# Optimization experiments

Measured on AMD Instinct MI355X. Metric: run time of the kernel, lower is better.

Reference implementation:

```python
import jax, jax.numpy as jnp
import numpy as np


def pfaffian(A):
    """Pfaffian of even-dim skew-symmetric A via Parlett-Reid LTL^T (no pivoting).
    pf(A) = prod over elimination steps of the (k, k+1) pivot."""
    n = A.shape[0]
    ar = jnp.arange(n)

    def step(carry, i):
        A, pf = carry
        k = 2 * i
        pivot = A[k, k + 1]
        mask = ar > (k + 1)                      # rows/cols k+2:
        tau = jnp.where(mask, A[k, :], 0.0) / pivot
        col = jnp.where(mask, A[:, k + 1], 0.0)
        # rank-2 skew update of the trailing submatrix
        A = A + tau[:, None] * col[None, :] - col[:, None] * tau[None, :]
        return (A, pf * pivot), None

    (A, pf), _ = jax.lax.scan(step, (A, jnp.ones((), A.dtype)), jnp.arange(n // 2))
    return pf


def setup_inputs() -> dict:
    key = jax.random.key(0)
    k1, k2 = jax.random.split(key)
    N = 128          # nsites; Nparticle = N (spin system, one particle per site)
    B = 128          # batch of Monte-Carlo configurations
    x = jax.random.normal(k1, (B, N), jnp.float32)
    scale = np.float32(np.sqrt(np.e / N))
    F = jax.random.normal(k2, (N * (2 * N - 1),), jnp.float32) * scale
    return {"x": x, "F": F}


def reference(x, F):
    N = x.shape[-1]
    Nparticle = N
    twoN = 2 * N
    # scatter parameter vector into strict lower triangle, antisymmetrize
    F_full = jnp.zeros((twoN, twoN), F.dtype).at[jnp.tril_indices(twoN, -1)].set(F)
    F_full = F_full - F_full.T

    def single(xi):
        # spin system: up orbitals where x>0, down orbitals where x<=0
        occ = jnp.concatenate([xi > 0, xi <= 0])
        idx = jnp.flatnonzero(occ, size=Nparticle)
        A = F_full[idx[:, None], idx[None, :]]   # [Nparticle, Nparticle] gather
        return pfaffian(A)

    return jax.vmap(single)(x)
```

## Files before the change

### kernel.cpp

```cpp
#include <hip/hip_runtime.h>


#define POFF(i) ((i) + (((i) >> 5) << 2))
#define RL(v, l) __int_as_float(__builtin_amdgcn_readlane(__float_as_int(v), (l)))

__global__ __launch_bounds__(512) void pfaffian_kernel(
    const float* __restrict__ x,
    const float* __restrict__ F,
    float* __restrict__ out)
{
    const int b    = blockIdx.x;
    const int t    = threadIdx.x;
    const int lane = t & 63;
    const int wave = t >> 6;

    __shared__ int idx_sh[128];
    __shared__ int wtot[4];
    __shared__ __align__(16) float tauLDS[2][4][144];
    __shared__ __align__(16) float colLDS[2][4][144];
    __shared__ __align__(16) float rS[2][4][144];
    __shared__ __align__(16) float cS[2][4][144];

    if (t < 256) {
        const float xv  = x[b * 128 + (t & 127)];
        const bool  pos = xv > 0.0f;
        const bool  o   = (t < 128) ? pos : !pos;
        const unsigned long long mm = __ballot(o);
        const int rank = __popcll(mm & ((1ull << lane) - 1ull));
        if (lane == 63) wtot[wave] = rank + (o ? 1 : 0);
        __syncthreads();
        int off = 0;
#pragma unroll
        for (int w = 0; w < 4; ++w)
            if (w < wave) off += wtot[w];
        if (o) idx_sh[off + rank] = t;
    } else {
        __syncthreads();
    }
    __syncthreads();

    const int rg   = t >> 4;
    const int cg   = t & 15;
    const int row0 = rg << 2;
    const int col0 = cg << 3;
    const int prow = POFF(row0);
    const int pcol = POFF(col0);

    int ri[4], ci[8];
#pragma unroll
    for (int a = 0; a < 4; ++a) ri[a] = idx_sh[row0 + a];
#pragma unroll
    for (int c = 0; c < 8; ++c) ci[c] = idx_sh[col0 + c];

    float A[4][8];
#pragma unroll
    for (int a = 0; a < 4; ++a) {
        const int ii = ri[a];
#pragma unroll
        for (int c = 0; c < 8; ++c) {
            const int jj = ci[c];
            const int hi = ii > jj ? ii : jj;
            const int lo = ii > jj ? jj : ii;
            float v = (ii == jj) ? 0.0f : F[(hi * (hi - 1)) / 2 + lo];
            A[a][c] = (ii < jj) ? -v : v;
        }
    }

    auto stage = [&](int Pn, int st) {
        const int rgbase = 2 * Pn;
        if (rg == rgbase) {
            *(float4*)&rS[st][0][pcol]     = make_float4(A[0][0], A[0][1], A[0][2], A[0][3]);
            *(float4*)&rS[st][0][pcol + 4] = make_float4(A[0][4], A[0][5], A[0][6], A[0][7]);
            *(float4*)&rS[st][1][pcol]     = make_float4(A[2][0], A[2][1], A[2][2], A[2][3]);
            *(float4*)&rS[st][1][pcol + 4] = make_float4(A[2][4], A[2][5], A[2][6], A[2][7]);
        }
        if (rg == rgbase + 1) {
            *(float4*)&rS[st][2][pcol]     = make_float4(A[0][0], A[0][1], A[0][2], A[0][3]);
            *(float4*)&rS[st][2][pcol + 4] = make_float4(A[0][4], A[0][5], A[0][6], A[0][7]);
            *(float4*)&rS[st][3][pcol]     = make_float4(A[2][0], A[2][1], A[2][2], A[2][3]);
            *(float4*)&rS[st][3][pcol + 4] = make_float4(A[2][4], A[2][5], A[2][6], A[2][7]);
        }
        if (cg == Pn) {
            *(float4*)&cS[st][0][prow] = make_float4(A[0][1], A[1][1], A[2][1], A[3][1]);
            *(float4*)&cS[st][1][prow] = make_float4(A[0][3], A[1][3], A[2][3], A[3][3]);
            *(float4*)&cS[st][2][prow] = make_float4(A[0][5], A[1][5], A[2][5], A[3][5]);
            *(float4*)&cS[st][3][prow] = make_float4(A[0][7], A[1][7], A[2][7], A[3][7]);
        }
    };
    stage(0, 0);
    stage(1, 1);
    __syncthreads();

    float pf = 1.0f;

    auto crew2 = [&](int Pn, bool pre) {
        const int sv = Pn & 1;
        const int g0 = lane << 1;
        const int g1 = g0 + 1;
        const int pg = POFF(g0);
        float R[4][2], C[4][2];
#pragma unroll
        for (int j = 0; j < 4; ++j) {
            const float2 rv = *(const float2*)&rS[sv][j][pg];
            const float2 cv = *(const float2*)&cS[sv][j][pg];
            R[j][0] = rv.x; R[j][1] = rv.y;
            C[j][0] = cv.x; C[j][1] = cv.y;
        }
        if (pre) {
            const int svp  = sv ^ 1;
            const int base = POFF(8 * Pn);
            float4 Tq[4][2], Cq[4][2];
#pragma unroll
            for (int jp = 0; jp < 4; ++jp) {
                Tq[jp][0] = *(const float4*)&tauLDS[svp][jp][base];
                Tq[jp][1] = *(const float4*)&tauLDS[svp][jp][base + 4];
                Cq[jp][0] = *(const float4*)&colLDS[svp][jp][base];
                Cq[jp][1] = *(const float4*)&colLDS[svp][jp][base + 4];
            }
#pragma unroll
            for (int jp = 0; jp < 4; ++jp) {
                const float trA[4] = {Tq[jp][0].x, Tq[jp][0].z, Tq[jp][1].x, Tq[jp][1].z};
                const float crA[4] = {Cq[jp][0].x, Cq[jp][0].z, Cq[jp][1].x, Cq[jp][1].z};
                const float tcA[4] = {Tq[jp][0].y, Tq[jp][0].w, Tq[jp][1].y, Tq[jp][1].w};
                const float ccA[4] = {Cq[jp][0].y, Cq[jp][0].w, Cq[jp][1].y, Cq[jp][1].w};
                const float2 tpv = *(const float2*)&tauLDS[svp][jp][pg];
                const float2 cpv = *(const float2*)&colLDS[svp][jp][pg];
#pragma unroll
                for (int a = 0; a < 4; ++a) {
                    const float tau_r = trA[a];
                    const float col_r = crA[a];
                    R[a][0] = __fmaf_rn(-col_r, tpv.x,
                              __fmaf_rn(tau_r, cpv.x, R[a][0]));
                    R[a][1] = __fmaf_rn(-col_r, tpv.y,
                              __fmaf_rn(tau_r, cpv.y, R[a][1]));
                    const float tau_c = tcA[a];
                    const float col_c = ccA[a];
                    C[a][0] = __fmaf_rn(-cpv.x, tau_c,
                              __fmaf_rn(tpv.x, col_c, C[a][0]));
                    C[a][1] = __fmaf_rn(-cpv.y, tau_c,
                              __fmaf_rn(tpv.y, col_c, C[a][1]));
                }
            }
        }
        float TAU[4][2], CV[4][2];
#pragma unroll
        for (int j = 0; j < 4; ++j) {
            const int k = 8 * Pn + 2 * j;
            const float piv = RL(R[j][1], 4 * Pn + j);
            pf = __fmul_rn(pf, piv);
            TAU[j][0] = (g0 > k + 1) ? __fdiv_rn(R[j][0], piv) : 0.0f;
            TAU[j][1] = (g1 > k + 1) ? __fdiv_rn(R[j][1], piv) : 0.0f;
            CV[j][0]  = (g0 > k + 1) ? C[j][0] : 0.0f;
            CV[j][1]  = (g1 > k + 1) ? C[j][1] : 0.0f;
            *(float2*)&tauLDS[sv][j][pg] = make_float2(TAU[j][0], TAU[j][1]);
            *(float2*)&colLDS[sv][j][pg] = make_float2(CV[j][0], CV[j][1]);
#pragma unroll
            for (int j2 = j + 1; j2 < 4; ++j2) {
                const int ls = 4 * Pn + j2;
                const float tau_r = RL(TAU[j][0], ls);
                const float col_r = RL(CV[j][0], ls);
                R[j2][0] = __fmaf_rn(-col_r, TAU[j][0],
                           __fmaf_rn(tau_r, CV[j][0], R[j2][0]));
                R[j2][1] = __fmaf_rn(-col_r, TAU[j][1],
                           __fmaf_rn(tau_r, CV[j][1], R[j2][1]));
                const float tau_c = RL(TAU[j][1], ls);
                const float col_c = RL(CV[j][1], ls);
                C[j2][0] = __fmaf_rn(-CV[j][0], tau_c,
                           __fmaf_rn(TAU[j][0], col_c, C[j2][0]));
                C[j2][1] = __fmaf_rn(-CV[j][1], tau_c,
                           __fmaf_rn(TAU[j][1], col_c, C[j2][1]));
            }
        }
    };

    if (wave == 0) crew2(0, false);
    __syncthreads();

    for (int P = 0; P < 15; ++P) {
        if (wave >= 1 && 2 * wave > P) {
            const int sp = P & 1;
#pragma unroll
            for (int j = 0; j < 4; ++j) {
                const float4 trv = *(const float4*)&tauLDS[sp][j][prow];
                const float4 crv = *(const float4*)&colLDS[sp][j][prow];
                const float4 t0v = *(const float4*)&tauLDS[sp][j][pcol];
                const float4 t1v = *(const float4*)&tauLDS[sp][j][pcol + 4];
                const float4 c0v = *(const float4*)&colLDS[sp][j][pcol];
                const float4 c1v = *(const float4*)&colLDS[sp][j][pcol + 4];
                const float tr[4] = {trv.x, trv.y, trv.z, trv.w};
                const float cr[4] = {crv.x, crv.y, crv.z, crv.w};
                const float tc[8] = {t0v.x, t0v.y, t0v.z, t0v.w,
                                     t1v.x, t1v.y, t1v.z, t1v.w};
                const float cc[8] = {c0v.x, c0v.y, c0v.z, c0v.w,
                                     c1v.x, c1v.y, c1v.z, c1v.w};
#pragma unroll
                for (int a = 0; a < 4; ++a) {
#pragma unroll
                    for (int c = 0; c < 8; ++c) {
                        A[a][c] = __fmaf_rn(-cr[a], tc[c],
                                  __fmaf_rn(tr[a], cc[c], A[a][c]));
                    }
                }
            }
            if (P <= 13) stage(P + 2, P & 1);
        }
        if (wave == 0) crew2(P + 1, true);
        __syncthreads();
    }

    if (t == 0) out[b] = pf;
}

extern "C" void kernel_launch(void* const* d_in, const int* in_sizes, int n_in,
                              void* d_out, int out_size, void* d_ws, size_t ws_size,
                              hipStream_t stream) {
    const float* x = (const float*)d_in[0];
    const float* F = (const float*)d_in[1];
    float* out     = (float*)d_out;
    (void)in_sizes; (void)n_in; (void)out_size; (void)d_ws; (void)ws_size;

    pfaffian_kernel<<<128, 512, 0, stream>>>(x, F, out);
}
```

Baseline: 76.55 us.

## Double the panel width to eight pivots per barrier step

Widens each elimination panel from 4 to 8 pivot steps (16 columns), so the outer loop runs 7 barrier-separated iterations instead of 15. Shared staging buffers, the panel-factor routine in wave 0, and the trailing rank-2k update all process 8 tau/col vectors per step. This is meant to cut the number of __syncthreads and the per-step latency overhead. In exchange the serial panel work in wave 0 grows (more readlane chains and divisions) and more trailing work falls into whichever waves remain active.

```diff
diff --git a/kernel.cpp b/kernel.cpp
--- a/kernel.cpp
+++ b/kernel.cpp
@@ -16,10 +16,10 @@
 
     __shared__ int idx_sh[128];
     __shared__ int wtot[4];
-    __shared__ __align__(16) float tauLDS[2][4][144];
-    __shared__ __align__(16) float colLDS[2][4][144];
-    __shared__ __align__(16) float rS[2][4][144];
-    __shared__ __align__(16) float cS[2][4][144];
+    __shared__ __align__(16) float tauLDS[2][8][144];
+    __shared__ __align__(16) float colLDS[2][8][144];
+    __shared__ __align__(16) float rS[2][8][144];
+    __shared__ __align__(16) float cS[2][8][144];
 
     if (t < 256) {
         const float xv  = x[b * 128 + (t & 127)];
@@ -67,24 +67,24 @@
     }
 
     auto stage = [&](int Pn, int st) {
-        const int rgbase = 2 * Pn;
-        if (rg == rgbase) {
-            *(float4*)&rS[st][0][pcol]     = make_float4(A[0][0], A[0][1], A[0][2], A[0][3]);
-            *(float4*)&rS[st][0][pcol + 4] = make_float4(A[0][4], A[0][5], A[0][6], A[0][7]);
-            *(float4*)&rS[st][1][pcol]     = make_float4(A[2][0], A[2][1], A[2][2], A[2][3]);
-            *(float4*)&rS[st][1][pcol + 4] = make_float4(A[2][4], A[2][5], A[2][6], A[2][7]);
-        }
-        if (rg == rgbase + 1) {
-            *(float4*)&rS[st][2][pcol]     = make_float4(A[0][0], A[0][1], A[0][2], A[0][3]);
-            *(float4*)&rS[st][2][pcol + 4] = make_float4(A[0][4], A[0][5], A[0][6], A[0][7]);
-            *(float4*)&rS[st][3][pcol]     = make_float4(A[2][0], A[2][1], A[2][2], A[2][3]);
-            *(float4*)&rS[st][3][pcol + 4] = make_float4(A[2][4], A[2][5], A[2][6], A[2][7]);
-        }
-        if (cg == Pn) {
+        const int q = rg - 4 * Pn;
+        if (q >= 0 && q < 4) {
+            *(float4*)&rS[st][2 * q][pcol]         = make_float4(A[0][0], A[0][1], A[0][2], A[0][3]);
+            *(float4*)&rS[st][2 * q][pcol + 4]     = make_float4(A[0][4], A[0][5], A[0][6], A[0][7]);
+            *(float4*)&rS[st][2 * q + 1][pcol]     = make_float4(A[2][0], A[2][1], A[2][2], A[2][3]);
+            *(float4*)&rS[st][2 * q + 1][pcol + 4] = make_float4(A[2][4], A[2][5], A[2][6], A[2][7]);
+        }
+        if (cg == 2 * Pn) {
             *(float4*)&cS[st][0][prow] = make_float4(A[0][1], A[1][1], A[2][1], A[3][1]);
             *(float4*)&cS[st][1][prow] = make_float4(A[0][3], A[1][3], A[2][3], A[3][3]);
             *(float4*)&cS[st][2][prow] = make_float4(A[0][5], A[1][5], A[2][5], A[3][5]);
             *(float4*)&cS[st][3][prow] = make_float4(A[0][7], A[1][7], A[2][7], A[3][7]);
+        }
+        if (cg == 2 * Pn + 1) {
+            *(float4*)&cS[st][4][prow] = make_float4(A[0][1], A[1][1], A[2][1], A[3][1]);
+            *(float4*)&cS[st][5][prow] = make_float4(A[0][3], A[1][3], A[2][3], A[3][3]);
+            *(float4*)&cS[st][6][prow] = make_float4(A[0][5], A[1][5], A[2][5], A[3][5]);
+            *(float4*)&cS[st][7][prow] = make_float4(A[0][7], A[1][7], A[2][7], A[3][7]);
         }
     };
     stage(0, 0);
@@ -98,9 +98,9 @@
         const int g0 = lane << 1;
         const int g1 = g0 + 1;
         const int pg = POFF(g0);
-        float R[4][2], C[4][2];
-#pragma unroll
-        for (int j = 0; j < 4; ++j) {
+        float R[8][2], C[8][2];
+#pragma unroll
+        for (int j = 0; j < 8; ++j) {
             const float2 rv = *(const float2*)&rS[sv][j][pg];
             const float2 cv = *(const float2*)&cS[sv][j][pg];
             R[j][0] = rv.x; R[j][1] = rv.y;
@@ -108,25 +108,25 @@
         }
         if (pre) {
             const int svp  = sv ^ 1;
-            const int base = POFF(8 * Pn);
-            float4 Tq[4][2], Cq[4][2];
-#pragma unroll
-            for (int jp = 0; jp < 4; ++jp) {
-                Tq[jp][0] = *(const float4*)&tauLDS[svp][jp][base];
-                Tq[jp][1] = *(const float4*)&tauLDS[svp][jp][base + 4];
-                Cq[jp][0] = *(const float4*)&colLDS[svp][jp][base];
-                Cq[jp][1] = *(const float4*)&colLDS[svp][jp][base + 4];
-            }
-#pragma unroll
-            for (int jp = 0; jp < 4; ++jp) {
-                const float trA[4] = {Tq[jp][0].x, Tq[jp][0].z, Tq[jp][1].x, Tq[jp][1].z};
-                const float crA[4] = {Cq[jp][0].x, Cq[jp][0].z, Cq[jp][1].x, Cq[jp][1].z};
-                const float tcA[4] = {Tq[jp][0].y, Tq[jp][0].w, Tq[jp][1].y, Tq[jp][1].w};
-                const float ccA[4] = {Cq[jp][0].y, Cq[jp][0].w, Cq[jp][1].y, Cq[jp][1].w};
+            const int base = POFF(16 * Pn);
+#pragma unroll
+            for (int jp = 0; jp < 8; ++jp) {
+                const float4 T0 = *(const float4*)&tauLDS[svp][jp][base];
+                const float4 T1 = *(const float4*)&tauLDS[svp][jp][base + 4];
+                const float4 T2 = *(const float4*)&tauLDS[svp][jp][base + 8];
+                const float4 T3 = *(const float4*)&tauLDS[svp][jp][base + 12];
+                const float4 D0 = *(const float4*)&colLDS[svp][jp][base];
+                const float4 D1 = *(const float4*)&colLDS[svp][jp][base + 4];
+                const float4 D2 = *(const float4*)&colLDS[svp][jp][base + 8];
+                const float4 D3 = *(const float4*)&colLDS[svp][jp][base + 12];
+                const float trA[8] = {T0.x, T0.z, T1.x, T1.z, T2.x, T2.z, T3.x, T3.z};
+                const float tcA[8] = {T0.y, T0.w, T1.y, T1.w, T2.y, T2.w, T3.y, T3.w};
+                const float crA[8] = {D0.x, D0.z, D1.x, D1.z, D2.x, D2.z, D3.x, D3.z};
+                const float ccA[8] = {D0.y, D0.w, D1.y, D1.w, D2.y, D2.w, D3.y, D3.w};
                 const float2 tpv = *(const float2*)&tauLDS[svp][jp][pg];
                 const float2 cpv = *(const float2*)&colLDS[svp][jp][pg];
 #pragma unroll
-                for (int a = 0; a < 4; ++a) {
+                for (int a = 0; a < 8; ++a) {
                     const float tau_r = trA[a];
                     const float col_r = crA[a];
                     R[a][0] = __fmaf_rn(-col_r, tpv.x,
@@ -142,11 +142,11 @@
                 }
             }
         }
-        float TAU[4][2], CV[4][2];
-#pragma unroll
-        for (int j = 0; j < 4; ++j) {
-            const int k = 8 * Pn + 2 * j;
-            const float piv = RL(R[j][1], 4 * Pn + j);
+        float TAU[8][2], CV[8][2];
+#pragma unroll
+        for (int j = 0; j < 8; ++j) {
+            const int k = 16 * Pn + 2 * j;
+            const float piv = RL(R[j][1], 8 * Pn + j);
             pf = __fmul_rn(pf, piv);
             TAU[j][0] = (g0 > k + 1) ? __fdiv_rn(R[j][0], piv) : 0.0f;
             TAU[j][1] = (g1 > k + 1) ? __fdiv_rn(R[j][1], piv) : 0.0f;
@@ -155,8 +155,8 @@
             *(float2*)&tauLDS[sv][j][pg] = make_float2(TAU[j][0], TAU[j][1]);
             *(float2*)&colLDS[sv][j][pg] = make_float2(CV[j][0], CV[j][1]);
 #pragma unroll
-            for (int j2 = j + 1; j2 < 4; ++j2) {
-                const int ls = 4 * Pn + j2;
+            for (int j2 = j + 1; j2 < 8; ++j2) {
+                const int ls = 8 * Pn + j2;
                 const float tau_r = RL(TAU[j][0], ls);
                 const float col_r = RL(CV[j][0], ls);
                 R[j2][0] = __fmaf_rn(-col_r, TAU[j][0],
@@ -176,11 +176,11 @@
     if (wave == 0) crew2(0, false);
     __syncthreads();
 
-    for (int P = 0; P < 15; ++P) {
-        if (wave >= 1 && 2 * wave > P) {
+    for (int P = 0; P < 7; ++P) {
+        if (wave >= P + 2) {
             const int sp = P & 1;
 #pragma unroll
-            for (int j = 0; j < 4; ++j) {
+            for (int j = 0; j < 8; ++j) {
                 const float4 trv = *(const float4*)&tauLDS[sp][j][prow];
                 const float4 crv = *(const float4*)&colLDS[sp][j][prow];
                 const float4 t0v = *(const float4*)&tauLDS[sp][j][pcol];
@@ -202,7 +202,7 @@
                     }
                 }
             }
-            if (P <= 13) stage(P + 2, P & 1);
+            if (P <= 5) stage(P + 2, P & 1);
         }
         if (wave == 0) crew2(P + 1, true);
         __syncthreads();
```

Result: slower. 78.27 us (+2.2%).

## Remap waves to row tiles and let wave 0 gather pivot panels directly

Applied to the files above, without the earlier changes.

Wave 0 no longer holds a tile of A. It gathers the first two pivot row and column panels straight from F into LDS, which removes the initial staging pass and one barrier. The other waves are remapped so that wave m owns row tiles via m = 8-wave or wave-3, and the loop's active condition now uses m instead of wave. The aim is to balance the trailing-update work across waves and overlap the startup gather, at the cost of more complex indexing and a risk of dropping coverage for rows that wave 0 used to own.

```diff
diff --git a/kernel.cpp b/kernel.cpp
--- a/kernel.cpp
+++ b/kernel.cpp
@@ -39,30 +39,43 @@
     }
     __syncthreads();
 
-    const int rg   = t >> 4;
+    const int m = (wave == 0) ? 0 : (wave <= 3 ? 8 - wave : wave - 3);
+
+    const int rg   = (m << 2) | ((t >> 4) & 3);
     const int cg   = t & 15;
     const int row0 = rg << 2;
     const int col0 = cg << 3;
     const int prow = POFF(row0);
     const int pcol = POFF(col0);
 
-    int ri[4], ci[8];
-#pragma unroll
-    for (int a = 0; a < 4; ++a) ri[a] = idx_sh[row0 + a];
-#pragma unroll
-    for (int c = 0; c < 8; ++c) ci[c] = idx_sh[col0 + c];
+    auto Fval = [&](int gi, int gj) -> float {
+        const int ii = idx_sh[gi];
+        const int jj = idx_sh[gj];
+        if (ii == jj) return 0.0f;
+        const int hi = ii > jj ? ii : jj;
+        const int lo = ii > jj ? jj : ii;
+        const float v = F[(hi * (hi - 1)) / 2 + lo];
+        return (ii < jj) ? -v : v;
+    };
 
     float A[4][8];
-#pragma unroll
-    for (int a = 0; a < 4; ++a) {
-        const int ii = ri[a];
-#pragma unroll
-        for (int c = 0; c < 8; ++c) {
-            const int jj = ci[c];
-            const int hi = ii > jj ? ii : jj;
-            const int lo = ii > jj ? jj : ii;
-            float v = (ii == jj) ? 0.0f : F[(hi * (hi - 1)) / 2 + lo];
-            A[a][c] = (ii < jj) ? -v : v;
+    if (wave >= 1) {
+        int ri[4], ci[8];
+#pragma unroll
+        for (int a = 0; a < 4; ++a) ri[a] = idx_sh[row0 + a];
+#pragma unroll
+        for (int c = 0; c < 8; ++c) ci[c] = idx_sh[col0 + c];
+#pragma unroll
+        for (int a = 0; a < 4; ++a) {
+            const int ii = ri[a];
+#pragma unroll
+            for (int c = 0; c < 8; ++c) {
+                const int jj = ci[c];
+                const int hi = ii > jj ? ii : jj;
+                const int lo = ii > jj ? jj : ii;
+                float v = (ii == jj) ? 0.0f : F[(hi * (hi - 1)) / 2 + lo];
+                A[a][c] = (ii < jj) ? -v : v;
+            }
         }
     }
 
@@ -87,9 +100,6 @@
             *(float4*)&cS[st][3][prow] = make_float4(A[0][7], A[1][7], A[2][7], A[3][7]);
         }
     };
-    stage(0, 0);
-    stage(1, 1);
-    __syncthreads();
 
     float pf = 1.0f;
 
@@ -173,11 +183,29 @@
         }
     };
 
-    if (wave == 0) crew2(0, false);
+    if (wave == 0) {
+        const int c0 = lane << 1;
+        const int pc = POFF(c0);
+#pragma unroll
+        for (int st = 0; st < 2; ++st) {
+#pragma unroll
+            for (int j = 0; j < 4; ++j) {
+                const int k = 8 * st + 2 * j;
+                float2 rv, cv;
+                rv.x = Fval(k, c0);
+                rv.y = Fval(k, c0 + 1);
+                cv.x = Fval(c0, k + 1);
+                cv.y = Fval(c0 + 1, k + 1);
+                *(float2*)&rS[st][j][pc] = rv;
+                *(float2*)&cS[st][j][pc] = cv;
+            }
+        }
+        crew2(0, false);
+    }
     __syncthreads();
 
     for (int P = 0; P < 15; ++P) {
-        if (wave >= 1 && 2 * wave > P) {
+        if (wave >= 1 && P < 2 * m) {
             const int sp = P & 1;
 #pragma unroll
             for (int j = 0; j < 4; ++j) {
```

Result: no change. 77.10 us (+0.7%).
